# Performance work log

Hardware: AMD Instinct MI355X
Metric: run time of the kernel (lower is better)

Reference implementation:

```python
import jax, jax.numpy as jnp
import numpy as np
from jax import lax

EPOCHS = 3
N_IN, N_OUT = 20, 18
BN_EPS = 1e-5
RECT_EPS = 1e-4
TRIU = np.triu_indices(N_OUT)  # SPDVectorize upper-triangular indices


def _orth(key, n, m):
    # Stiefel init: orthonormal columns, like nn.init.orthogonal_
    q, _ = jnp.linalg.qr(jax.random.normal(key, (n, m), dtype=jnp.float32))
    return q


def setup_inputs() -> dict:
    key = jax.random.key(0)
    ks = jax.random.split(key, 8)
    bs = 2048
    f32 = jnp.float32
    return dict(
        x=jax.random.normal(ks[0], (bs, 1, 22, 438), dtype=f32),
        W1=jax.random.normal(ks[1], (22, 1, 22, 1), dtype=f32) * 0.1,
        b1=jnp.zeros((22,), f32),
        g1=jnp.ones((22,), f32), be1=jnp.zeros((22,), f32),
        W2=jax.random.normal(ks[2], (20, 22, 1, 12), dtype=f32) * 0.05,
        b2=jnp.zeros((20,), f32),
        g2=jnp.ones((20,), f32), be2=jnp.zeros((20,), f32),
        Wq=_orth(ks[3], N_IN, N_OUT),
        Wk=_orth(ks[4], N_IN, N_OUT),
        Wv=_orth(ks[5], N_IN, N_OUT),
        Wl=jax.random.normal(ks[6], (N_OUT * (N_OUT + 1) // 2 * EPOCHS, 4), dtype=f32) * 0.02,
        bl=jnp.zeros((4,), f32),
    )


def _bn(x, g, b):
    # BatchNorm2d forward in training mode (batch statistics, biased var)
    mean = x.mean(axis=(0, 2, 3), keepdims=True)
    var = ((x - mean) ** 2).mean(axis=(0, 2, 3), keepdims=True)
    return (x - mean) * lax.rsqrt(var + BN_EPS) * g[None, :, None, None] + b[None, :, None, None]


def _conv(x, w, b, pad_w):
    y = lax.conv_general_dilated(x, w, (1, 1), [(0, 0), (pad_w, pad_w)],
                                 dimension_numbers=('NCHW', 'OIHW', 'NCHW'))
    return y + b[None, :, None, None]


def _signal2spd(x):
    # x: (bs, C, L) -> trace-normalized covariance + 1e-5 * I
    L = x.shape[-1]
    xc = x - x.mean(-1, keepdims=True)
    cov = jnp.einsum('bcl,bdl->bcd', xc, xc) / (L - 1)
    cov = cov / jnp.trace(cov, axis1=-2, axis2=-1)[:, None, None]
    return cov + 1e-5 * jnp.eye(cov.shape[-1], dtype=cov.dtype)


def _patch_lens(n, epochs):
    base = n // epochs
    lens = [base] * epochs
    for i in range(n - base * epochs):
        lens[i] += 1
    return lens


def _spd_fn(t, fn):
    # SPD functional calculus via eigh (== torch.svd on SPD input)
    s, u = jnp.linalg.eigh(t)
    return jnp.einsum('...ij,...j,...kj->...ik', u, fn(s), u)


def _forward(x, W1, b1, g1, be1, W2, b2, g2, be2, Wq, Wk, Wv, Wl, bl):
    bs = x.shape[0]
    h = _bn(_conv(x, W1, b1, 0), g1, be1)          # (bs,22,1,438)
    h = _bn(_conv(h, W2, b2, 6), g2, be2)          # (bs,20,1,439)
    sig = h[:, :, 0, :]                            # squeeze -> (bs,20,439)
    covs, off = [], 0
    for L in _patch_lens(sig.shape[-1], EPOCHS):   # E2R: [147,146,146]
        covs.append(_signal2spd(sig[:, :, off:off + L]))
        off += L
    X = jnp.stack(covs, axis=1)                    # (bs,m,20,20) SPD
    # SPDTransform: W^T X W with Stiefel W (20,18)
    Q = jnp.einsum('pi,bmpq,qj->bmij', Wq, X, Wq)
    K = jnp.einsum('pi,bmpq,qj->bmij', Wk, X, Wk)
    V = jnp.einsum('pi,bmpq,qj->bmij', Wv, X, Wv)
    logQ = _spd_fn(Q, jnp.log)
    logK = _spd_fn(K, jnp.log)
    logV = _spd_fn(V, jnp.log)
    # log-Euclidean distance^2: ||log Q_j - log K_i||_F^2  (== sum of svd singvals of D D^T)
    diff = logQ[:, :, None] - logK[:, None, :]     # (bs, mq, mk, n, n)
    energy = jnp.sum(diff * diff, axis=(-2, -1))   # (bs, mq, mk)
    scores = 1.0 / (1.0 + jnp.log1p(energy))
    # torch: softmax over dim=-2 then permute(0,2,1) == softmax over K index here
    P = jax.nn.softmax(scores, axis=-1)            # (bs, mq, mk)
    mixed = jnp.einsum('bji,bipq->bjpq', P, logV)  # weighted log-Euclidean mean
    out = _spd_fn(mixed, jnp.exp)
    out = _spd_fn(out, lambda s: jnp.maximum(s, RECT_EPS))  # SPDRectified
    logO = _spd_fn(out, jnp.log)                   # SPDTangentSpace log
    vec = logO[..., TRIU[0], TRIU[1]]              # (bs, m, 171)
    return vec.reshape(bs, -1) @ Wl + bl           # (bs, 4)


def reference(x, W1, b1, g1, be1, W2, b2, g2, be2, Wq, Wk, Wv, Wl, bl):
    return _forward(x, W1, b1, g1, be1, W2, b2, g2, be2, Wq, Wk, Wv, Wl, bl)
```

## Files before the change

### kernel.cpp

```cpp
#include <hip/hip_runtime.h>
#include <math.h>

#define OFF_G3   0
#define OFF_QKV  17981440
#define OFF_ST   (17981440 + 5971968)
#define ST_SX   0
#define ST_SXX  22
#define ST_WF   506
#define ST_BF   990
#define ST_Y2S  1012
#define ST_Y2Q  1032
#define ST_TOT  1052

#define LOGEPS -9.210340371976182f
#define NSWEEP 5
#define SHIFT  12.0f

__global__ __launch_bounds__(256) void k0_zero(float* __restrict__ st){
  for (int i = threadIdx.x; i < ST_TOT; i += 256) st[i] = 0.f;
}

__global__ __launch_bounds__(256) void k1_xstats(const float* __restrict__ x, float* __restrict__ st){
  __shared__ __align__(16) float xs[22*444];
  const float* xb = x + (size_t)blockIdx.x * (22*438);
  for (int i = threadIdx.x; i < 22*444; i += 256){
    int h = i / 444, w = i - h*444;
    xs[i] = (w < 438) ? xb[h*438 + w] : 0.f;
  }
  __syncthreads();
  for (int t = threadIdx.x; t < 275; t += 256){
    if (t < 22){
      const float4* r = (const float4*)&xs[t*444];
      float4 acc = {0.f,0.f,0.f,0.f};
      for (int w = 0; w < 111; ++w){ float4 v = r[w]; acc.x+=v.x; acc.y+=v.y; acc.z+=v.z; acc.w+=v.w; }
      atomicAdd(&st[ST_SX + t], acc.x+acc.y+acc.z+acc.w);
    } else {
      int rem = t - 22, h = 0;
      while (rem >= 22 - h){ rem -= 22 - h; ++h; }
      int h2 = h + rem;
      const float4* ra = (const float4*)&xs[h*444];
      const float4* rb = (const float4*)&xs[h2*444];
      float4 acc = {0.f,0.f,0.f,0.f};
      for (int w = 0; w < 111; ++w){
        float4 a = ra[w], b = rb[w];
        acc.x = fmaf(a.x,b.x,acc.x); acc.y = fmaf(a.y,b.y,acc.y);
        acc.z = fmaf(a.z,b.z,acc.z); acc.w = fmaf(a.w,b.w,acc.w);
      }
      atomicAdd(&st[ST_SXX + h*22 + h2], acc.x+acc.y+acc.z+acc.w);
    }
  }
}

__global__ __launch_bounds__(64) void k1b_fold(const float* __restrict__ W1, const float* __restrict__ g1,
                                               const float* __restrict__ be1, float* __restrict__ st){
  int c = threadIdx.x;
  if (c >= 22) return;
  const float invN = 1.f / (2048.f*438.f);
  float mcol[22];
  float mu0 = 0.f;
  for (int h = 0; h < 22; ++h){ mcol[h] = W1[c*22 + h]; mu0 = fmaf(mcol[h], st[ST_SX + h], mu0); }
  mu0 *= invN;
  float qf = 0.f;
  for (int h = 0; h < 22; ++h)
    for (int h2 = h; h2 < 22; ++h2){
      float w = mcol[h]*mcol[h2]*st[ST_SXX + h*22 + h2];
      qf += (h2 == h) ? w : 2.f*w;
    }
  qf *= invN;
  float var = qf - mu0*mu0;
  float a1 = g1[c] * rsqrtf(var + 1e-5f);
  for (int h = 0; h < 22; ++h) st[ST_WF + h*22 + c] = a1 * mcol[h];
  st[ST_BF + c] = be1[c] - a1 * mu0;
}

__global__ __launch_bounds__(256) void k2_weff(const float* __restrict__ W2, const float* __restrict__ st,
                                               float* __restrict__ weff2, float* __restrict__ pfx){
  __shared__ float wf[484];
  __shared__ float bf[22];
  for (int i = threadIdx.x; i < 484; i += 256) wf[i] = st[ST_WF + i];
  if (threadIdx.x < 22) bf[threadIdx.x] = st[ST_BF + threadIdx.x];
  __syncthreads();
  for (int i = threadIdx.x; i < 5280; i += 256){
    int t = i % 12; int tmp = i / 12;
    int dl = tmp % 5; tmp /= 5;
    int h = tmp % 22; int dg = tmp / 22;
    int d = dg*5 + dl;
    float a = 0.f;
    for (int c = 0; c < 22; ++c) a = fmaf(W2[d*264 + c*12 + t], wf[h*22 + c], a);
    weff2[i] = a;
  }
  if (threadIdx.x < 20){
    int d = threadIdx.x;
    float run = 0.f;
    pfx[d*13 + 0] = 0.f;
    for (int t = 0; t < 12; ++t){
      float a = 0.f;
      for (int c = 0; c < 22; ++c) a = fmaf(W2[d*264 + c*12 + t], bf[c], a);
      run += a;
      pfx[d*13 + t + 1] = run;
    }
  }
}

__global__ __launch_bounds__(512, 3) void k3_convg(const float* __restrict__ x,
    const float* __restrict__ weff2, const float* __restrict__ pfx,
    float* __restrict__ st, float* __restrict__ g3o){
  __shared__ __align__(16) float smem[10304];
  float* ps   = smem + 9944;
  float* sloc = smem + 10204;
  float* qloc = smem + 10224;
  float* mus  = smem + 10244;
  int tid = threadIdx.x;
  int n = blockIdx.x;
  const float* xb = x + (size_t)n*9636;
  for (int i = tid; i < 22*452; i += 512){
    int h = i / 452, w = i - h*452;
    int gx = w - 6;
    smem[i] = (gx >= 0 && gx < 438) ? xb[h*438 + gx] : 0.f;
  }
  if (tid < 260) ps[tid] = pfx[tid];
  if (tid < 40){ if (tid < 20) sloc[tid] = 0.f; else qloc[tid-20] = 0.f; }
  __syncthreads();
  int wave = tid >> 6;
  int dg = __builtin_amdgcn_readfirstlane(wave >> 1);
  int ct = tid & 127;
  bool act = ct < 110;
  int c0 = act ? ct*4 : 0;
  float acc[5][4];
  #pragma unroll
  for (int dl = 0; dl < 5; ++dl)
    #pragma unroll
    for (int j = 0; j < 4; ++j) acc[dl][j] = 0.f;
  const float* wb = weff2 + dg*1320;
  #pragma unroll 1
  for (int h = 0; h < 22; ++h){
    const float4* xr = (const float4*)&smem[h*452 + c0];
    float4 v0 = xr[0], v1 = xr[1], v2 = xr[2], v3 = xr[3];
    float xw[16] = {v0.x,v0.y,v0.z,v0.w, v1.x,v1.y,v1.z,v1.w,
                    v2.x,v2.y,v2.z,v2.w, v3.x,v3.y,v3.z,v3.w};
    const float* wp = wb + h*60;
    #pragma unroll
    for (int dl = 0; dl < 5; ++dl){
      #pragma unroll
      for (int t = 0; t < 12; ++t){
        float w = wp[dl*12 + t];
        #pragma unroll
        for (int j = 0; j < 4; ++j)
          acc[dl][j] = fmaf(w, xw[t+j], acc[dl][j]);
      }
    }
  }
  float s5[5], q5[5];
  #pragma unroll
  for (int dl = 0; dl < 5; ++dl){ s5[dl] = 0.f; q5[dl] = 0.f; }
  if (act){
    #pragma unroll
    for (int dl = 0; dl < 5; ++dl){
      int d = dg*5 + dl;
      #pragma unroll
      for (int j = 0; j < 4; ++j){
        int gw = c0 + j;
        if (gw < 439){
          int lo = 6 - gw; if (lo < 0) lo = 0;
          int hi = 444 - gw; if (hi > 12) hi = 12;
          float val = acc[dl][j] + (ps[d*13 + hi] - ps[d*13 + lo]);
          acc[dl][j] = val;
          s5[dl] += val; q5[dl] = fmaf(val, val, q5[dl]);
        }
      }
    }
  }
  #pragma unroll
  for (int off = 32; off; off >>= 1){
    #pragma unroll
    for (int dl = 0; dl < 5; ++dl){
      s5[dl] += __shfl_down(s5[dl], off);
      q5[dl] += __shfl_down(q5[dl], off);
    }
  }
  if ((tid & 63) == 0){
    #pragma unroll
    for (int dl = 0; dl < 5; ++dl){
      atomicAdd(&sloc[dg*5 + dl], s5[dl]);
      atomicAdd(&qloc[dg*5 + dl], q5[dl]);
    }
  }
  __syncthreads();
  if (tid < 20){
    atomicAdd(&st[ST_Y2S + tid], sloc[tid]);
    atomicAdd(&st[ST_Y2Q + tid], qloc[tid]);
  }
  if (act){
    #pragma unroll
    for (int dl = 0; dl < 5; ++dl){
      int d = dg*5 + dl;
      #pragma unroll
      for (int j = 0; j < 4; ++j){
        int gw = c0 + j;
        if (gw < 439){
          int m = (gw >= 293) ? 2 : ((gw >= 147) ? 1 : 0);
          int lw = gw - ((m == 2) ? 293 : ((m == 1) ? 147 : 0));
          smem[m*2960 + d*148 + lw] = acc[dl][j];
        }
      }
    }
  }
  if (tid < 100){
    int d = tid/5, k = tid - d*5;
    int m = (k == 0) ? 0 : ((k < 3) ? 1 : 2);
    int lw = (k == 0) ? 147 : ((k == 1 || k == 3) ? 146 : 147);
    smem[m*2960 + d*148 + lw] = 0.f;
  }
  __syncthreads();
  if (tid < 60){
    int m = tid/20, d = tid - m*20;
    const float4* r = (const float4*)&smem[m*2960 + d*148];
    float4 a4 = {0.f,0.f,0.f,0.f};
    #pragma unroll 1
    for (int w = 0; w < 37; ++w){ float4 v = r[w]; a4.x+=v.x; a4.y+=v.y; a4.z+=v.z; a4.w+=v.w; }
    mus[tid] = a4.x+a4.y+a4.z+a4.w;
  }
  __syncthreads();
  for (int it = tid; it < 630; it += 512){
    int m = it/210, t = it - m*210;
    int rem = t, c = 0;
    while (rem >= 20 - c){ rem -= 20 - c; ++c; }
    int d = c + rem;
    const float4* ra = (const float4*)&smem[m*2960 + c*148];
    const float4* rb = (const float4*)&smem[m*2960 + d*148];
    float4 acc4 = {0.f,0.f,0.f,0.f};
    #pragma unroll 1
    for (int w = 0; w < 37; ++w){
      float4 a = ra[w], b = rb[w];
      acc4.x = fmaf(a.x,b.x,acc4.x); acc4.y = fmaf(a.y,b.y,acc4.y);
      acc4.z = fmaf(a.z,b.z,acc4.z); acc4.w = fmaf(a.w,b.w,acc4.w);
    }
    float invL = (m == 0) ? (1.f/147.f) : (1.f/146.f);
    float a = (acc4.x+acc4.y+acc4.z+acc4.w) - mus[m*20+c]*mus[m*20+d]*invL;
    float* gm = g3o + (size_t)n*1200 + m*400;
    gm[c*20 + d] = a; gm[d*20 + c] = a;
  }
}

__global__ __launch_bounds__(256) void k4_qkv(const float* __restrict__ g3i, const float* __restrict__ st,
    const float* __restrict__ g2, const float* __restrict__ Wq, const float* __restrict__ Wk,
    const float* __restrict__ Wv, float* __restrict__ qkv){
  __shared__ __align__(16) float G3[3][400];
  __shared__ float a2s[20];
  __shared__ __align__(16) float Bt[3][18][20];
  __shared__ __align__(16) float Tmt[3][360];
  __shared__ float rtr3[3];
  int tid = threadIdx.x, n = blockIdx.x;
  if (tid < 20){
    const float invN = 1.f/(2048.f*439.f);
    float s = st[ST_Y2S + tid]*invN;
    float q = st[ST_Y2Q + tid]*invN;
    a2s[tid] = g2[tid] * rsqrtf(q - s*s + 1e-5f);
  }
  const float* gi = g3i + (size_t)n*1200;
  for (int i = tid; i < 1200; i += 256) (&G3[0][0])[i] = gi[i];
  __syncthreads();
  for (int i = tid; i < 1080; i += 256){
    int wt = i/360, r = i - wt*360; int d = r/18, jj = r - d*18;
    const float* Wm = (wt==0) ? Wq : ((wt==1) ? Wk : Wv);
    Bt[wt][jj][d] = a2s[d]*Wm[d*18 + jj];
  }
  __syncthreads();
  for (int wt = 0; wt < 3; ++wt){
    for (int i = tid; i < 1083; i += 256){
      if (i < 1080){
        int m = i/360, r = i - m*360; int p = r/18, jj = r - p*18;
        const float4* gr = (const float4*)&G3[m][p*20];
        const float4* br = (const float4*)&Bt[wt][jj][0];
        float4 a4 = {0.f,0.f,0.f,0.f};
        #pragma unroll
        for (int w = 0; w < 5; ++w){
          float4 a = gr[w], b = br[w];
          a4.x = fmaf(a.x,b.x,a4.x); a4.y = fmaf(a.y,b.y,a4.y);
          a4.z = fmaf(a.z,b.z,a4.z); a4.w = fmaf(a.w,b.w,a4.w);
        }
        Tmt[m][jj*20 + p] = a4.x+a4.y+a4.z+a4.w;
      } else if (wt == 0){
        int m = i - 1080;
        float tr = 0.f;
        for (int c = 0; c < 20; ++c){ float a = a2s[c]; tr = fmaf(a*a, G3[m][c*21], tr); }
        rtr3[m] = 1.f/tr;
      }
    }
    __syncthreads();
    for (int it = tid; it < 513; it += 256){
      int m = it/171, t = it - m*171;
      int rem = t, i = 0;
      while (rem >= 18 - i){ rem -= 18 - i; ++i; }
      int jj = i + rem;
      const float4* br = (const float4*)&Bt[wt][i][0];
      const float4* tr = (const float4*)&Tmt[m][jj*20];
      float4 a4 = {0.f,0.f,0.f,0.f};
      #pragma unroll
      for (int w = 0; w < 5; ++w){
        float4 a = br[w], b = tr[w];
        a4.x = fmaf(a.x,b.x,a4.x); a4.y = fmaf(a.y,b.y,a4.y);
        a4.z = fmaf(a.z,b.z,a4.z); a4.w = fmaf(a.w,b.w,a4.w);
      }
      float acc = (a4.x+a4.y+a4.z+a4.w) * rtr3[m];
      if (i == jj) acc += 1e-5f;
      float* outm = qkv + ((size_t)wt*6144 + (size_t)n*3 + m)*324;
      outm[i*18 + jj] = acc; outm[jj*18 + i] = acc;
    }
    __syncthreads();
  }
}

__global__ __launch_bounds__(256, 4) void k5_oneside(const float* __restrict__ src, float* __restrict__ dst,
    int nmat, int mode, const float* __restrict__ Wl, const float* __restrict__ bl,
    float* __restrict__ outp){
  __shared__ __align__(16) float stage[12][384];
  __shared__ __align__(16) float wls[2052];
  __shared__ float outacc[4][4];
  int tid = threadIdx.x;
  int wave = tid >> 6, lane = tid & 63;
  int g = (lane >= 54) ? 3 : (lane >= 36 ? 2 : (lane >= 18 ? 1 : 0));
  int j = lane - g*18;
  int gb = g*18;
  int slot = wave*3 + ((g < 3) ? g : 0);
  int mat = blockIdx.x*12 + wave*3 + g;
  bool act = (g < 3) && (mat < nmat);

  if (mode == 1){
    for (int i = tid; i < 2052; i += 256) wls[i] = Wl[i];
    if (tid < 16) outacc[tid >> 2][tid & 3] = 0.f;
  }

  float b[18];
  float sh = (mode == 1) ? SHIFT : 0.f;
  if (act){
    const float* s = src + (size_t)mat*324 + j*18;
    #pragma unroll
    for (int i = 0; i < 18; ++i) b[i] = s[i] + ((i == j) ? sh : 0.f);
  } else {
    #pragma unroll
    for (int i = 0; i < 18; ++i) b[i] = (i == j) ? 1.f : 0.f;
  }
  float nrm;
  { float n0 = 0.f, n1 = 0.f;
    #pragma unroll
    for (int k = 0; k < 18; k += 2){ n0 = fmaf(b[k],b[k],n0); n1 = fmaf(b[k+1],b[k+1],n1); }
    nrm = n0 + n1; }

  #pragma unroll 1
  for (int sweep = 0; sweep < NSWEEP; ++sweep){
    #pragma unroll
    for (int r = 0; r < 17; ++r){
      int xx = j - 1 - r; if (xx < 0) xx += 17;
      int v = r + 17 - xx; if (v >= 17) v -= 17;
      int m = (j == 0) ? (1 + r) : ((xx == 0) ? 0 : (1 + v));
      bool isp = (j == 0) ? true : ((xx == 0) ? false : (xx <= 8));
      int plane = (gb + m) & 63;
      float rv[18];
      #pragma unroll
      for (int k = 0; k < 18; ++k) rv[k] = __shfl(b[k], plane);
      float on = __shfl(nrm, plane);
      float g0 = 0.f, g1 = 0.f;
      #pragma unroll
      for (int k = 0; k < 18; k += 2){ g0 = fmaf(b[k], rv[k], g0); g1 = fmaf(b[k+1], rv[k+1], g1); }
      float gam = g0 + g1;
      float alpha = isp ? nrm : on;
      float beta  = isp ? on  : nrm;
      float tau = (beta - alpha) * 0.5f * __builtin_amdgcn_rcpf(gam);
      float tt = __builtin_amdgcn_rcpf(fabsf(tau) + sqrtf(fmaf(tau, tau, 1.f)));
      float t = (tau >= 0.f) ? tt : -tt;
      if (!(fabsf(gam) > 1e-36f)) t = 0.f;
      float c = __builtin_amdgcn_rsqf(fmaf(t, t, 1.f));
      float s = t*c;
      nrm = fmaf(isp ? -t : t, gam, nrm);
      float sg = isp ? -s : s;
      #pragma unroll
      for (int k = 0; k < 18; ++k) b[k] = fmaf(c, b[k], sg*rv[k]);
    }
  }
  float n0 = 0.f, n1 = 0.f;
  #pragma unroll
  for (int k = 0; k < 18; k += 2){ n0 = fmaf(b[k],b[k],n0); n1 = fmaf(b[k+1],b[k+1],n1); }
  float nf = fmaxf(n0 + n1, 1e-30f);
  float fv = (mode == 0) ? (0.5f * logf(nf)) : fmaxf(sqrtf(nf) - SHIFT, LOGEPS);
  float wv = fv * __builtin_amdgcn_rcpf(nf);
  float* sp = &stage[slot][0];
  if (act){
    #pragma unroll
    for (int k = 0; k < 18; ++k) sp[k*20 + j] = b[k];
    sp[360 + j] = wv;
  }
  __syncthreads();
  if (act){
    float wr[18];
    #pragma unroll
    for (int i = 0; i < 18; ++i) wr[i] = sp[j*20 + i] * sp[360 + i];
    float frow[18];
    #pragma unroll
    for (int i2 = 0; i2 < 18; ++i2){
      const float* br = &sp[i2*20];
      float a0 = 0.f;
      #pragma unroll
      for (int k = 0; k < 16; k += 4){
        float4 v4 = *(const float4*)&br[k];
        a0 = fmaf(wr[k],   v4.x, a0); a0 = fmaf(wr[k+1], v4.y, a0);
        a0 = fmaf(wr[k+2], v4.z, a0); a0 = fmaf(wr[k+3], v4.w, a0);
      }
      a0 = fmaf(wr[16], br[16], a0);
      a0 = fmaf(wr[17], br[17], a0);
      frow[i2] = a0;
    }
    if (mode == 0){
      float* orow = dst + (size_t)mat*324 + j*18;
      #pragma unroll
      for (int i2 = 0; i2 < 18; ++i2) orow[i2] = frow[i2];
    } else {
      int base = (g*171 + j*(37 - j)/2 - j)*4;
      float o0=0.f, o1=0.f, o2=0.f, o3=0.f;
      #pragma unroll
      for (int jj = 0; jj < 18; ++jj){
        if (jj >= j){
          const float* w4 = &wls[base + jj*4];
          o0 = fmaf(frow[jj], w4[0], o0);
          o1 = fmaf(frow[jj], w4[1], o1);
          o2 = fmaf(frow[jj], w4[2], o2);
          o3 = fmaf(frow[jj], w4[3], o3);
        }
      }
      atomicAdd(&outacc[wave][0], o0);
      atomicAdd(&outacc[wave][1], o1);
      atomicAdd(&outacc[wave][2], o2);
      atomicAdd(&outacc[wave][3], o3);
    }
  }
  if (mode == 1){
    __syncthreads();
    if (tid < 16){
      int bi = tid >> 2, o = tid & 3;
      outp[(blockIdx.x*4 + bi)*4 + o] = outacc[bi][o] + bl[o];
    }
  }
}

__global__ __launch_bounds__(128) void k6_attnmix(const float* __restrict__ logs, float* __restrict__ mixed){
  __shared__ float lq[972], lk[972], lv[972];
  __shared__ float ew[2][9];
  __shared__ float P[9];
  int b = blockIdx.x, tid = threadIdx.x;
  const float* q  = logs + (size_t)b*972;
  const float* k_ = logs + 1990656 + (size_t)b*972;
  const float* v_ = logs + 3981312 + (size_t)b*972;
  for (int i = tid; i < 972; i += 128){ lq[i] = q[i]; lk[i] = k_[i]; lv[i] = v_[i]; }
  __syncthreads();
  float e[9] = {0.f,0.f,0.f,0.f,0.f,0.f,0.f,0.f,0.f};
  for (int x = tid; x < 324; x += 128){
    float q0 = lq[x], q1 = lq[324+x], q2 = lq[648+x];
    float k0 = lk[x], k1 = lk[324+x], k2 = lk[648+x];
    float d;
    d = q0-k0; e[0] = fmaf(d,d,e[0]);
    d = q0-k1; e[1] = fmaf(d,d,e[1]);
    d = q0-k2; e[2] = fmaf(d,d,e[2]);
    d = q1-k0; e[3] = fmaf(d,d,e[3]);
    d = q1-k1; e[4] = fmaf(d,d,e[4]);
    d = q1-k2; e[5] = fmaf(d,d,e[5]);
    d = q2-k0; e[6] = fmaf(d,d,e[6]);
    d = q2-k1; e[7] = fmaf(d,d,e[7]);
    d = q2-k2; e[8] = fmaf(d,d,e[8]);
  }
  #pragma unroll
  for (int p = 0; p < 9; ++p)
    for (int off = 32; off; off >>= 1) e[p] += __shfl_down(e[p], off);
  if ((tid & 63) == 0){
    #pragma unroll
    for (int p = 0; p < 9; ++p) ew[tid >> 6][p] = e[p];
  }
  __syncthreads();
  if (tid < 3){
    float en0 = ew[0][tid*3+0] + ew[1][tid*3+0];
    float en1 = ew[0][tid*3+1] + ew[1][tid*3+1];
    float en2 = ew[0][tid*3+2] + ew[1][tid*3+2];
    float s0 = 1.f/(1.f + log1pf(en0));
    float s1 = 1.f/(1.f + log1pf(en1));
    float s2 = 1.f/(1.f + log1pf(en2));
    float mx = fmaxf(s0, fmaxf(s1, s2));
    float e0 = expf(s0-mx), e1 = expf(s1-mx), e2 = expf(s2-mx);
    float inv = 1.f/(e0+e1+e2);
    P[tid*3+0] = e0*inv; P[tid*3+1] = e1*inv; P[tid*3+2] = e2*inv;
  }
  __syncthreads();
  float p00=P[0],p01=P[1],p02=P[2],p10=P[3],p11=P[4],p12=P[5],p20=P[6],p21=P[7],p22=P[8];
  float* mb = mixed + (size_t)b*972;
  for (int x = tid; x < 324; x += 128){
    float v0 = lv[x], v1 = lv[324+x], v2 = lv[648+x];
    mb[x]     = p00*v0 + p01*v1 + p02*v2;
    mb[324+x] = p10*v0 + p11*v1 + p12*v2;
    mb[648+x] = p20*v0 + p21*v1 + p22*v2;
  }
}

extern "C" void kernel_launch(void* const* d_in, const int* in_sizes, int n_in,
                              void* d_out, int out_size, void* d_ws, size_t ws_size,
                              hipStream_t stream){
  (void)in_sizes; (void)n_in; (void)out_size; (void)ws_size;
  const float* x   = (const float*)d_in[0];
  const float* W1  = (const float*)d_in[1];
  const float* g1  = (const float*)d_in[3];
  const float* be1 = (const float*)d_in[4];
  const float* W2  = (const float*)d_in[5];
  const float* g2  = (const float*)d_in[7];
  const float* Wq  = (const float*)d_in[9];
  const float* Wk  = (const float*)d_in[10];
  const float* Wv  = (const float*)d_in[11];
  const float* Wl  = (const float*)d_in[12];
  const float* bl  = (const float*)d_in[13];
  float* ws    = (float*)d_ws;
  float* g3buf = ws + OFF_G3;
  float* qkv   = ws + OFF_QKV;
  float* weff2 = ws + OFF_QKV;
  float* pfx   = ws + OFF_QKV + 5280;
  float* logs  = ws + OFF_G3;
  float* mixed = ws + OFF_QKV;
  float* st    = ws + OFF_ST;
  float* outp  = (float*)d_out;

  k0_zero    <<<dim3(1),       dim3(256), 0, stream>>>(st);
  k1_xstats  <<<dim3(2048),    dim3(256), 0, stream>>>(x, st);
  k1b_fold   <<<dim3(1),       dim3(64),  0, stream>>>(W1, g1, be1, st);
  k2_weff    <<<dim3(1),       dim3(256), 0, stream>>>(W2, st, weff2, pfx);
  k3_convg   <<<dim3(2048),    dim3(512), 0, stream>>>(x, weff2, pfx, st, g3buf);
  k4_qkv     <<<dim3(2048),    dim3(256), 0, stream>>>(g3buf, st, g2, Wq, Wk, Wv, qkv);
  k5_oneside <<<dim3(1536),    dim3(256), 0, stream>>>(qkv, logs, 18432, 0, nullptr, nullptr, nullptr);
  k6_attnmix <<<dim3(2048),    dim3(128), 0, stream>>>(logs, mixed);
  k5_oneside <<<dim3(512),     dim3(256), 0, stream>>>(mixed, nullptr, 6144, 1, Wl, bl, outp);
}
```

Baseline: 695.3 us.

## Fuse QKV projection, eigen-logs, attention mix and final eig into one kernel

Replaces the k4_qkv, k5_oneside (twice) and k6_attnmix launches with a single per-sample 192-thread kernel that keeps the Q/K/V matrices, their logs and the mixed result in shared memory. This removes the global-memory round trips of the qkv, logs and mixed buffers and three kernel launches. The cost is that the second Jacobi eigensolve runs only on wave 0 while the other two waves return and sit idle. The per-block shared-memory footprint and the block shape also change.

```diff
diff --git a/kernel.cpp b/kernel.cpp
--- a/kernel.cpp
+++ b/kernel.cpp
@@ -242,111 +242,7 @@
   }
 }
 
-__global__ __launch_bounds__(256) void k4_qkv(const float* __restrict__ g3i, const float* __restrict__ st,
-    const float* __restrict__ g2, const float* __restrict__ Wq, const float* __restrict__ Wk,
-    const float* __restrict__ Wv, float* __restrict__ qkv){
-  __shared__ __align__(16) float G3[3][400];
-  __shared__ float a2s[20];
-  __shared__ __align__(16) float Bt[3][18][20];
-  __shared__ __align__(16) float Tmt[3][360];
-  __shared__ float rtr3[3];
-  int tid = threadIdx.x, n = blockIdx.x;
-  if (tid < 20){
-    const float invN = 1.f/(2048.f*439.f);
-    float s = st[ST_Y2S + tid]*invN;
-    float q = st[ST_Y2Q + tid]*invN;
-    a2s[tid] = g2[tid] * rsqrtf(q - s*s + 1e-5f);
-  }
-  const float* gi = g3i + (size_t)n*1200;
-  for (int i = tid; i < 1200; i += 256) (&G3[0][0])[i] = gi[i];
-  __syncthreads();
-  for (int i = tid; i < 1080; i += 256){
-    int wt = i/360, r = i - wt*360; int d = r/18, jj = r - d*18;
-    const float* Wm = (wt==0) ? Wq : ((wt==1) ? Wk : Wv);
-    Bt[wt][jj][d] = a2s[d]*Wm[d*18 + jj];
-  }
-  __syncthreads();
-  for (int wt = 0; wt < 3; ++wt){
-    for (int i = tid; i < 1083; i += 256){
-      if (i < 1080){
-        int m = i/360, r = i - m*360; int p = r/18, jj = r - p*18;
-        const float4* gr = (const float4*)&G3[m][p*20];
-        const float4* br = (const float4*)&Bt[wt][jj][0];
-        float4 a4 = {0.f,0.f,0.f,0.f};
-        #pragma unroll
-        for (int w = 0; w < 5; ++w){
-          float4 a = gr[w], b = br[w];
-          a4.x = fmaf(a.x,b.x,a4.x); a4.y = fmaf(a.y,b.y,a4.y);
-          a4.z = fmaf(a.z,b.z,a4.z); a4.w = fmaf(a.w,b.w,a4.w);
-        }
-        Tmt[m][jj*20 + p] = a4.x+a4.y+a4.z+a4.w;
-      } else if (wt == 0){
-        int m = i - 1080;
-        float tr = 0.f;
-        for (int c = 0; c < 20; ++c){ float a = a2s[c]; tr = fmaf(a*a, G3[m][c*21], tr); }
-        rtr3[m] = 1.f/tr;
-      }
-    }
-    __syncthreads();
-    for (int it = tid; it < 513; it += 256){
-      int m = it/171, t = it - m*171;
-      int rem = t, i = 0;
-      while (rem >= 18 - i){ rem -= 18 - i; ++i; }
-      int jj = i + rem;
-      const float4* br = (const float4*)&Bt[wt][i][0];
-      const float4* tr = (const float4*)&Tmt[m][jj*20];
-      float4 a4 = {0.f,0.f,0.f,0.f};
-      #pragma unroll
-      for (int w = 0; w < 5; ++w){
-        float4 a = br[w], b = tr[w];
-        a4.x = fmaf(a.x,b.x,a4.x); a4.y = fmaf(a.y,b.y,a4.y);
-        a4.z = fmaf(a.z,b.z,a4.z); a4.w = fmaf(a.w,b.w,a4.w);
-      }
-      float acc = (a4.x+a4.y+a4.z+a4.w) * rtr3[m];
-      if (i == jj) acc += 1e-5f;
-      float* outm = qkv + ((size_t)wt*6144 + (size_t)n*3 + m)*324;
-      outm[i*18 + jj] = acc; outm[jj*18 + i] = acc;
-    }
-    __syncthreads();
-  }
-}
-
-__global__ __launch_bounds__(256, 4) void k5_oneside(const float* __restrict__ src, float* __restrict__ dst,
-    int nmat, int mode, const float* __restrict__ Wl, const float* __restrict__ bl,
-    float* __restrict__ outp){
-  __shared__ __align__(16) float stage[12][384];
-  __shared__ __align__(16) float wls[2052];
-  __shared__ float outacc[4][4];
-  int tid = threadIdx.x;
-  int wave = tid >> 6, lane = tid & 63;
-  int g = (lane >= 54) ? 3 : (lane >= 36 ? 2 : (lane >= 18 ? 1 : 0));
-  int j = lane - g*18;
-  int gb = g*18;
-  int slot = wave*3 + ((g < 3) ? g : 0);
-  int mat = blockIdx.x*12 + wave*3 + g;
-  bool act = (g < 3) && (mat < nmat);
-
-  if (mode == 1){
-    for (int i = tid; i < 2052; i += 256) wls[i] = Wl[i];
-    if (tid < 16) outacc[tid >> 2][tid & 3] = 0.f;
-  }
-
-  float b[18];
-  float sh = (mode == 1) ? SHIFT : 0.f;
-  if (act){
-    const float* s = src + (size_t)mat*324 + j*18;
-    #pragma unroll
-    for (int i = 0; i < 18; ++i) b[i] = s[i] + ((i == j) ? sh : 0.f);
-  } else {
-    #pragma unroll
-    for (int i = 0; i < 18; ++i) b[i] = (i == j) ? 1.f : 0.f;
-  }
-  float nrm;
-  { float n0 = 0.f, n1 = 0.f;
-    #pragma unroll
-    for (int k = 0; k < 18; k += 2){ n0 = fmaf(b[k],b[k],n0); n1 = fmaf(b[k+1],b[k+1],n1); }
-    nrm = n0 + n1; }
-
+__device__ __forceinline__ void jacobi_sweeps(float b[18], float& nrm, int j, int gb){
   #pragma unroll 1
   for (int sweep = 0; sweep < NSWEEP; ++sweep){
     #pragma unroll
@@ -378,84 +274,144 @@
       for (int k = 0; k < 18; ++k) b[k] = fmaf(c, b[k], sg*rv[k]);
     }
   }
-  float n0 = 0.f, n1 = 0.f;
-  #pragma unroll
-  for (int k = 0; k < 18; k += 2){ n0 = fmaf(b[k],b[k],n0); n1 = fmaf(b[k+1],b[k+1],n1); }
-  float nf = fmaxf(n0 + n1, 1e-30f);
-  float fv = (mode == 0) ? (0.5f * logf(nf)) : fmaxf(sqrtf(nf) - SHIFT, LOGEPS);
-  float wv = fv * __builtin_amdgcn_rcpf(nf);
-  float* sp = &stage[slot][0];
+}
+
+__global__ __launch_bounds__(192, 4) void k5_mega(const float* __restrict__ g3i,
+    const float* __restrict__ st, const float* __restrict__ g2,
+    const float* __restrict__ Wq, const float* __restrict__ Wk, const float* __restrict__ Wv,
+    const float* __restrict__ Wl, const float* __restrict__ bl, float* __restrict__ outp){
+  __shared__ __align__(16) float S[3456];
+  __shared__ __align__(16) float L[2916];
+  __shared__ float a2s[20];
+  __shared__ float rtr3[3];
+  __shared__ float ew[3][9];
+  __shared__ float P[9];
+  int tid = threadIdx.x, n = blockIdx.x;
+  int wave = tid >> 6, lane = tid & 63;
+
+  float* G3s = S;
+  float* Bt  = S + 1200;
+  float* Tmt = S + 2280;
+  if (tid < 20){
+    const float invN = 1.f/(2048.f*439.f);
+    float s = st[ST_Y2S + tid]*invN;
+    float q = st[ST_Y2Q + tid]*invN;
+    a2s[tid] = g2[tid] * rsqrtf(q - s*s + 1e-5f);
+  }
+  const float* gi = g3i + (size_t)n*1200;
+  for (int i = tid; i < 1200; i += 192) G3s[i] = gi[i];
+  __syncthreads();
+  for (int i = tid; i < 1080; i += 192){
+    int wt = i/360, r = i - wt*360; int d = r/18, jj = r - d*18;
+    const float* Wm = (wt==0) ? Wq : ((wt==1) ? Wk : Wv);
+    Bt[wt*360 + jj*20 + d] = a2s[d]*Wm[d*18 + jj];
+  }
+  __syncthreads();
+  for (int wt = 0; wt < 3; ++wt){
+    for (int i = tid; i < 1083; i += 192){
+      if (i < 1080){
+        int m = i/360, r = i - m*360; int p = r/18, jj = r - p*18;
+        const float4* gr = (const float4*)&G3s[m*400 + p*20];
+        const float4* br = (const float4*)&Bt[wt*360 + jj*20];
+        float4 a4 = {0.f,0.f,0.f,0.f};
+        #pragma unroll
+        for (int w = 0; w < 5; ++w){
+          float4 a = gr[w], b = br[w];
+          a4.x = fmaf(a.x,b.x,a4.x); a4.y = fmaf(a.y,b.y,a4.y);
+          a4.z = fmaf(a.z,b.z,a4.z); a4.w = fmaf(a.w,b.w,a4.w);
+        }
+        Tmt[m*360 + jj*20 + p] = a4.x+a4.y+a4.z+a4.w;
+      } else if (wt == 0){
+        int m = i - 1080;
+        float tr = 0.f;
+        for (int c = 0; c < 20; ++c){ float a = a2s[c]; tr = fmaf(a*a, G3s[m*400 + c*21], tr); }
+        rtr3[m] = 1.f/tr;
+      }
+    }
+    __syncthreads();
+    for (int it = tid; it < 513; it += 192){
+      int m = it/171, t = it - m*171;
+      int rem = t, i = 0;
+      while (rem >= 18 - i){ rem -= 18 - i; ++i; }
+      int jj = i + rem;
+      const float4* br = (const float4*)&Bt[wt*360 + i*20];
+      const float4* tr = (const float4*)&Tmt[m*360 + jj*20];
+      float4 a4 = {0.f,0.f,0.f,0.f};
+      #pragma unroll
+      for (int w = 0; w < 5; ++w){
+        float4 a = br[w], b = tr[w];
+        a4.x = fmaf(a.x,b.x,a4.x); a4.y = fmaf(a.y,b.y,a4.y);
+        a4.z = fmaf(a.z,b.z,a4.z); a4.w = fmaf(a.w,b.w,a4.w);
+      }
+      float acc = (a4.x+a4.y+a4.z+a4.w) * rtr3[m];
+      if (i == jj) acc += 1e-5f;
+      float* Lm = L + wt*972 + m*324;
+      Lm[i*18 + jj] = acc; Lm[jj*18 + i] = acc;
+    }
+    __syncthreads();
+  }
+
+  int g = (lane >= 54) ? 3 : (lane >= 36 ? 2 : (lane >= 18 ? 1 : 0));
+  int j = lane - g*18;
+  int gb = g*18;
+  int slot = wave*3 + ((g < 3) ? g : 0);
+  bool act = (g < 3);
+  float b[18];
   if (act){
-    #pragma unroll
-    for (int k = 0; k < 18; ++k) sp[k*20 + j] = b[k];
-    sp[360 + j] = wv;
-  }
-  __syncthreads();
-  if (act){
-    float wr[18];
-    #pragma unroll
-    for (int i = 0; i < 18; ++i) wr[i] = sp[j*20 + i] * sp[360 + i];
-    float frow[18];
-    #pragma unroll
-    for (int i2 = 0; i2 < 18; ++i2){
-      const float* br = &sp[i2*20];
-      float a0 = 0.f;
-      #pragma unroll
-      for (int k = 0; k < 16; k += 4){
-        float4 v4 = *(const float4*)&br[k];
-        a0 = fmaf(wr[k],   v4.x, a0); a0 = fmaf(wr[k+1], v4.y, a0);
-        a0 = fmaf(wr[k+2], v4.z, a0); a0 = fmaf(wr[k+3], v4.w, a0);
-      }
-      a0 = fmaf(wr[16], br[16], a0);
-      a0 = fmaf(wr[17], br[17], a0);
-      frow[i2] = a0;
-    }
-    if (mode == 0){
-      float* orow = dst + (size_t)mat*324 + j*18;
-      #pragma unroll
-      for (int i2 = 0; i2 < 18; ++i2) orow[i2] = frow[i2];
-    } else {
-      int base = (g*171 + j*(37 - j)/2 - j)*4;
-      float o0=0.f, o1=0.f, o2=0.f, o3=0.f;
-      #pragma unroll
-      for (int jj = 0; jj < 18; ++jj){
-        if (jj >= j){
-          const float* w4 = &wls[base + jj*4];
-          o0 = fmaf(frow[jj], w4[0], o0);
-          o1 = fmaf(frow[jj], w4[1], o1);
-          o2 = fmaf(frow[jj], w4[2], o2);
-          o3 = fmaf(frow[jj], w4[3], o3);
+    const float* sc = &L[wave*972 + g*324 + j*18];
+    #pragma unroll
+    for (int i = 0; i < 18; ++i) b[i] = sc[i];
+  } else {
+    #pragma unroll
+    for (int i = 0; i < 18; ++i) b[i] = (i == j) ? 1.f : 0.f;
+  }
+  float nrm;
+  { float n0 = 0.f, n1 = 0.f;
+    #pragma unroll
+    for (int k = 0; k < 18; k += 2){ n0 = fmaf(b[k],b[k],n0); n1 = fmaf(b[k+1],b[k+1],n1); }
+    nrm = n0 + n1; }
+  jacobi_sweeps(b, nrm, j, gb);
+  { float n0 = 0.f, n1 = 0.f;
+    #pragma unroll
+    for (int k = 0; k < 18; k += 2){ n0 = fmaf(b[k],b[k],n0); n1 = fmaf(b[k+1],b[k+1],n1); }
+    float nf = fmaxf(n0 + n1, 1e-30f);
+    float fv = 0.5f * logf(nf);
+    float wv = fv * __builtin_amdgcn_rcpf(nf);
+    float* sp = &S[slot*384];
+    if (act){
+      #pragma unroll
+      for (int k = 0; k < 18; ++k) sp[k*20 + j] = b[k];
+      sp[360 + j] = wv;
+    }
+    __syncthreads();
+    if (act){
+      float wr[18];
+      #pragma unroll
+      for (int i = 0; i < 18; ++i) wr[i] = sp[j*20 + i] * sp[360 + i];
+      float* orow = &L[wave*972 + g*324 + j*18];
+      #pragma unroll
+      for (int i2 = 0; i2 < 18; ++i2){
+        const float* br = &sp[i2*20];
+        float a0 = 0.f;
+        #pragma unroll
+        for (int k = 0; k < 16; k += 4){
+          float4 v4 = *(const float4*)&br[k];
+          a0 = fmaf(wr[k],   v4.x, a0); a0 = fmaf(wr[k+1], v4.y, a0);
+          a0 = fmaf(wr[k+2], v4.z, a0); a0 = fmaf(wr[k+3], v4.w, a0);
         }
-      }
-      atomicAdd(&outacc[wave][0], o0);
-      atomicAdd(&outacc[wave][1], o1);
-      atomicAdd(&outacc[wave][2], o2);
-      atomicAdd(&outacc[wave][3], o3);
-    }
-  }
-  if (mode == 1){
-    __syncthreads();
-    if (tid < 16){
-      int bi = tid >> 2, o = tid & 3;
-      outp[(blockIdx.x*4 + bi)*4 + o] = outacc[bi][o] + bl[o];
-    }
-  }
-}
-
-__global__ __launch_bounds__(128) void k6_attnmix(const float* __restrict__ logs, float* __restrict__ mixed){
-  __shared__ float lq[972], lk[972], lv[972];
-  __shared__ float ew[2][9];
-  __shared__ float P[9];
-  int b = blockIdx.x, tid = threadIdx.x;
-  const float* q  = logs + (size_t)b*972;
-  const float* k_ = logs + 1990656 + (size_t)b*972;
-  const float* v_ = logs + 3981312 + (size_t)b*972;
-  for (int i = tid; i < 972; i += 128){ lq[i] = q[i]; lk[i] = k_[i]; lv[i] = v_[i]; }
-  __syncthreads();
+        a0 = fmaf(wr[16], br[16], a0);
+        a0 = fmaf(wr[17], br[17], a0);
+        orow[i2] = a0;
+      }
+    }
+  }
+  __syncthreads();
+
+  for (int i = tid; i < 2052; i += 192) S[i] = Wl[i];
   float e[9] = {0.f,0.f,0.f,0.f,0.f,0.f,0.f,0.f,0.f};
-  for (int x = tid; x < 324; x += 128){
-    float q0 = lq[x], q1 = lq[324+x], q2 = lq[648+x];
-    float k0 = lk[x], k1 = lk[324+x], k2 = lk[648+x];
+  for (int x = tid; x < 324; x += 192){
+    float q0 = L[x],     q1 = L[324+x],     q2 = L[648+x];
+    float k0 = L[972+x], k1 = L[1296+x],    k2 = L[1620+x];
     float d;
     d = q0-k0; e[0] = fmaf(d,d,e[0]);
     d = q0-k1; e[1] = fmaf(d,d,e[1]);
@@ -470,15 +426,15 @@
   #pragma unroll
   for (int p = 0; p < 9; ++p)
     for (int off = 32; off; off >>= 1) e[p] += __shfl_down(e[p], off);
-  if ((tid & 63) == 0){
-    #pragma unroll
-    for (int p = 0; p < 9; ++p) ew[tid >> 6][p] = e[p];
+  if (lane == 0){
+    #pragma unroll
+    for (int p = 0; p < 9; ++p) ew[wave][p] = e[p];
   }
   __syncthreads();
   if (tid < 3){
-    float en0 = ew[0][tid*3+0] + ew[1][tid*3+0];
-    float en1 = ew[0][tid*3+1] + ew[1][tid*3+1];
-    float en2 = ew[0][tid*3+2] + ew[1][tid*3+2];
+    float en0 = ew[0][tid*3+0] + ew[1][tid*3+0] + ew[2][tid*3+0];
+    float en1 = ew[0][tid*3+1] + ew[1][tid*3+1] + ew[2][tid*3+1];
+    float en2 = ew[0][tid*3+2] + ew[1][tid*3+2] + ew[2][tid*3+2];
     float s0 = 1.f/(1.f + log1pf(en0));
     float s1 = 1.f/(1.f + log1pf(en1));
     float s2 = 1.f/(1.f + log1pf(en2));
@@ -488,13 +444,65 @@
     P[tid*3+0] = e0*inv; P[tid*3+1] = e1*inv; P[tid*3+2] = e2*inv;
   }
   __syncthreads();
-  float p00=P[0],p01=P[1],p02=P[2],p10=P[3],p11=P[4],p12=P[5],p20=P[6],p21=P[7],p22=P[8];
-  float* mb = mixed + (size_t)b*972;
-  for (int x = tid; x < 324; x += 128){
-    float v0 = lv[x], v1 = lv[324+x], v2 = lv[648+x];
-    mb[x]     = p00*v0 + p01*v1 + p02*v2;
-    mb[324+x] = p10*v0 + p11*v1 + p12*v2;
-    mb[648+x] = p20*v0 + p21*v1 + p22*v2;
+  {
+    float p00=P[0],p01=P[1],p02=P[2],p10=P[3],p11=P[4],p12=P[5],p20=P[6],p21=P[7],p22=P[8];
+    for (int x = tid; x < 324; x += 192){
+      float v0 = L[1944+x], v1 = L[2268+x], v2 = L[2592+x];
+      L[x]     = p00*v0 + p01*v1 + p02*v2;
+      L[324+x] = p10*v0 + p11*v1 + p12*v2;
+      L[648+x] = p20*v0 + p21*v1 + p22*v2;
+    }
+  }
+  __syncthreads();
+
+  if (wave != 0) return;
+  float b2[18];
+  if (act){
+    const float* sc = &L[g*324 + j*18];
+    #pragma unroll
+    for (int i = 0; i < 18; ++i) b2[i] = sc[i] + ((i == j) ? SHIFT : 0.f);
+  } else {
+    #pragma unroll
+    for (int i = 0; i < 18; ++i) b2[i] = (i == j) ? 1.f : 0.f;
+  }
+  float nrm2;
+  { float n0 = 0.f, n1 = 0.f;
+    #pragma unroll
+    for (int k = 0; k < 18; k += 2){ n0 = fmaf(b2[k],b2[k],n0); n1 = fmaf(b2[k+1],b2[k+1],n1); }
+    nrm2 = n0 + n1; }
+  jacobi_sweeps(b2, nrm2, j, gb);
+  float o0 = 0.f, o1 = 0.f, o2 = 0.f, o3 = 0.f;
+  { float n0 = 0.f, n1 = 0.f;
+    #pragma unroll
+    for (int k = 0; k < 18; k += 2){ n0 = fmaf(b2[k],b2[k],n0); n1 = fmaf(b2[k+1],b2[k+1],n1); }
+    float nf = fmaxf(n0 + n1, 1e-30f);
+    float fv = fmaxf(sqrtf(nf) - SHIFT, LOGEPS);
+    float wv = fv * __builtin_amdgcn_rcpf(nf);
+    if (act){
+      #pragma unroll
+      for (int r = 0; r < 18; ++r){
+        float br = wv * b2[r];
+        int rowbase = (g*171 + r*(37 - r)/2 - r)*4;
+        #pragma unroll
+        for (int c = r; c < 18; ++c){
+          float f = br * b2[c];
+          const float* w4 = &S[rowbase + c*4];
+          o0 = fmaf(f, w4[0], o0); o1 = fmaf(f, w4[1], o1);
+          o2 = fmaf(f, w4[2], o2); o3 = fmaf(f, w4[3], o3);
+        }
+      }
+    }
+  }
+  #pragma unroll
+  for (int off = 32; off; off >>= 1){
+    o0 += __shfl_down(o0, off); o1 += __shfl_down(o1, off);
+    o2 += __shfl_down(o2, off); o3 += __shfl_down(o3, off);
+  }
+  if (lane == 0){
+    outp[n*4 + 0] = o0 + bl[0];
+    outp[n*4 + 1] = o1 + bl[1];
+    outp[n*4 + 2] = o2 + bl[2];
+    outp[n*4 + 3] = o3 + bl[3];
   }
 }
 
@@ -515,21 +523,15 @@
   const float* bl  = (const float*)d_in[13];
   float* ws    = (float*)d_ws;
   float* g3buf = ws + OFF_G3;
-  float* qkv   = ws + OFF_QKV;
   float* weff2 = ws + OFF_QKV;
   float* pfx   = ws + OFF_QKV + 5280;
-  float* logs  = ws + OFF_G3;
-  float* mixed = ws + OFF_QKV;
   float* st    = ws + OFF_ST;
   float* outp  = (float*)d_out;
 
-  k0_zero    <<<dim3(1),       dim3(256), 0, stream>>>(st);
-  k1_xstats  <<<dim3(2048),    dim3(256), 0, stream>>>(x, st);
-  k1b_fold   <<<dim3(1),       dim3(64),  0, stream>>>(W1, g1, be1, st);
-  k2_weff    <<<dim3(1),       dim3(256), 0, stream>>>(W2, st, weff2, pfx);
-  k3_convg   <<<dim3(2048),    dim3(512), 0, stream>>>(x, weff2, pfx, st, g3buf);
-  k4_qkv     <<<dim3(2048),    dim3(256), 0, stream>>>(g3buf, st, g2, Wq, Wk, Wv, qkv);
-  k5_oneside <<<dim3(1536),    dim3(256), 0, stream>>>(qkv, logs, 18432, 0, nullptr, nullptr, nullptr);
-  k6_attnmix <<<dim3(2048),    dim3(128), 0, stream>>>(logs, mixed);
-  k5_oneside <<<dim3(512),     dim3(256), 0, stream>>>(mixed, nullptr, 6144, 1, Wl, bl, outp);
-}
+  k0_zero    <<<dim3(1),    dim3(256), 0, stream>>>(st);
+  k1_xstats  <<<dim3(2048), dim3(256), 0, stream>>>(x, st);
+  k1b_fold   <<<dim3(1),    dim3(64),  0, stream>>>(W1, g1, be1, st);
+  k2_weff    <<<dim3(1),    dim3(256), 0, stream>>>(W2, st, weff2, pfx);
+  k3_convg   <<<dim3(2048), dim3(512), 0, stream>>>(x, weff2, pfx, st, g3buf);
+  k5_mega    <<<dim3(2048), dim3(192), 0, stream>>>(g3buf, st, g2, Wq, Wk, Wv, Wl, bl, outp);
+}
```

Result: no change. 700.4 us (+0.7%).
